# Kernel optimization log

Measured on AMD Instinct MI355X. Metric: run time of the kernel, lower is better.

The kernel has to match this reference:

```python
import jax, jax.numpy as jnp
import numpy as np

N_NODES = 100000
N_EDGES = 1600000
ATOM_EMB = 64
BOND_EMB = 16
MSG_DIM = 64
OUT_HIDDEN = 128
N_MOLS = 2048
MSG_PASSES = 4


def setup_inputs() -> dict:
    key = jax.random.key(0)
    ks = jax.random.split(key, 16)
    x = jax.random.randint(ks[0], (N_NODES,), 0, 119)
    edge_attr = jax.random.randint(ks[1], (N_EDGES,), 0, 4)
    edge_index = jax.random.randint(ks[2], (2, N_EDGES), 0, N_NODES)
    batch = jnp.sort(jax.random.randint(ks[3], (N_NODES,), 0, N_MOLS))
    s = 0.02
    atom_table = jax.random.normal(ks[4], (119, ATOM_EMB), jnp.float32) * s
    bond_table = jax.random.normal(ks[5], (4, BOND_EMB), jnp.float32) * s
    Wi = jax.random.normal(ks[6], (ATOM_EMB + BOND_EMB, MSG_DIM), jnp.float32) * s
    bi = jnp.zeros((MSG_DIM,), jnp.float32)
    Wu = jax.random.normal(ks[7], (ATOM_EMB + BOND_EMB + MSG_DIM, MSG_DIM), jnp.float32) * s
    bu = jnp.zeros((MSG_DIM,), jnp.float32)
    W1 = jax.random.normal(ks[8], (MSG_DIM, OUT_HIDDEN), jnp.float32) * s
    b1 = jnp.zeros((OUT_HIDDEN,), jnp.float32)
    W2 = jax.random.normal(ks[9], (OUT_HIDDEN, 1), jnp.float32) * s
    b2 = jnp.zeros((1,), jnp.float32)
    return {"x": x, "edge_attr": edge_attr, "edge_index": edge_index, "batch": batch,
            "atom_table": atom_table, "bond_table": bond_table,
            "Wi": Wi, "bi": bi, "Wu": Wu, "bu": bu,
            "W1": W1, "b1": b1, "W2": W2, "b2": b2}


def reference(x, edge_attr, edge_index, batch, atom_table, bond_table, Wi, bi, Wu, bu, W1, b1, W2, b2):
    atom = atom_table[x]                      # [N, ATOM_EMB]
    bond = bond_table[edge_attr]              # [E, BOND_EMB]
    src, dst = edge_index[0], edge_index[1]
    atom_src = atom[src]                      # [E, ATOM_EMB]
    ab = jnp.concatenate([atom_src, bond], axis=1)
    msg = jax.nn.relu(ab @ Wi + bi)           # [E, MSG_DIM]
    for _ in range(MSG_PASSES):
        agg = jax.ops.segment_sum(msg, dst, num_segments=N_NODES)  # [N, MSG_DIM]
        upd_in = jnp.concatenate([ab, agg[src]], axis=1)           # [E, 144]
        msg = jax.nn.relu(upd_in @ Wu + bu)
    node_state = jax.ops.segment_sum(msg, dst, num_segments=N_NODES)
    mol_state = jax.ops.segment_sum(node_state, batch, num_segments=N_MOLS)
    h = jax.nn.relu(mol_state @ W1 + b1)
    return (h @ W2 + b2).squeeze(-1)          # [N_MOLS]
```

## Files before the change

kernel.cpp:

```cpp
#include <hip/hip_runtime.h>

#define MSG 64
#define SLICE_SHIFT 10
#define MAXSLICES 128
#define CAP_E 20480
#define CAP_B 16384
#define NBIN 64

typedef _Float16 h2 __attribute__((ext_vector_type(2)));
typedef _Float16 h4 __attribute__((ext_vector_type(4)));
typedef _Float16 h8 __attribute__((ext_vector_type(8)));

__device__ inline h8 relu8(h8 v) {
    h8 z = {};
    return __builtin_elementwise_max(v, z);
}

__device__ inline h2 u2h(unsigned u) { union { unsigned u; h2 h; } c; c.u = u; return c.h; }

__global__ void build_tabA_kernel(const float* __restrict__ atom, const float* __restrict__ W,
                                  _Float16* __restrict__ tA, int rows) {
    int t = blockIdx.x * blockDim.x + threadIdx.x;
    if (t >= rows * MSG) return;
    int i = t & 63, a = t >> 6;
    float s = 0.f;
    for (int k = 0; k < 64; ++k) s = fmaf(atom[a * 64 + k], W[k * 64 + i], s);
    tA[t] = (_Float16)s;
}

__global__ void build_tabB_kernel(const float* __restrict__ bond, const float* __restrict__ W16,
                                  const float* __restrict__ bias, _Float16* __restrict__ tB) {
    int t = threadIdx.x;
    int i = t & 63, b = t >> 6;
    float s = bias[i];
    for (int k = 0; k < 16; ++k) s = fmaf(bond[b * 16 + k], W16[k * 64 + i], s);
    tB[t] = (_Float16)s;
}

__global__ void build_tabW_kernel(const float* __restrict__ W, unsigned* __restrict__ wst) {
    int t = blockIdx.x * 256 + threadIdx.x;
    if (t >= 2048) return;
    int k2 = t >> 6, c = t & 63;
    h2 h; h[0] = (_Float16)W[(2 * k2) * 64 + c]; h[1] = (_Float16)W[(2 * k2 + 1) * 64 + c];
    union { h2 h; unsigned u; } cv; cv.h = h;
    wst[k2 * 64 + c] = cv.u;
}

__global__ void node_init_kernel(const int* __restrict__ x, const _Float16* __restrict__ tA,
                                 _Float16* __restrict__ bufC, int N) {
    int t = blockIdx.x * blockDim.x + threadIdx.x;
    int v = t >> 3, j = t & 7;
    if (v < N) ((h8*)bufC)[(long long)v * 8 + j] = ((const h8*)tA)[x[v] * 8 + j];
}

__global__ void ginit_kernel(int* __restrict__ gcur, int K) {
    int s = blockIdx.x * blockDim.x + threadIdx.x;
    if (s < K) gcur[s] = s * CAP_E;
}

__global__ __launch_bounds__(256) void partition_kernel(
    const int* __restrict__ ei, const int* __restrict__ eattr,
    int E, int* __restrict__ gcur, unsigned long long* __restrict__ aux, int K)
{
    __shared__ int cnt[MAXSLICES];
    __shared__ int base[MAXSLICES];
    if (threadIdx.x < MAXSLICES) cnt[threadIdx.x] = 0;
    __syncthreads();
    int e0 = blockIdx.x * 1024;
    int sl0 = -1, sl1 = -1, sl2 = -1, sl3 = -1;
    int rk0 = 0, rk1 = 0, rk2 = 0, rk3 = 0;
    unsigned long long p0 = 0, p1 = 0, p2 = 0, p3 = 0;
    {
        int e = e0 + 0 * 256 + threadIdx.x;
        if (e < E) {
            int s = ei[e], d = ei[E + e];
            p0 = ((unsigned long long)((unsigned)s | ((unsigned)eattr[e] << 17)) << 17) | (unsigned)d;
            sl0 = d >> SLICE_SHIFT; rk0 = atomicAdd(&cnt[sl0], 1);
        }
    }
    {
        int e = e0 + 1 * 256 + threadIdx.x;
        if (e < E) {
            int s = ei[e], d = ei[E + e];
            p1 = ((unsigned long long)((unsigned)s | ((unsigned)eattr[e] << 17)) << 17) | (unsigned)d;
            sl1 = d >> SLICE_SHIFT; rk1 = atomicAdd(&cnt[sl1], 1);
        }
    }
    {
        int e = e0 + 2 * 256 + threadIdx.x;
        if (e < E) {
            int s = ei[e], d = ei[E + e];
            p2 = ((unsigned long long)((unsigned)s | ((unsigned)eattr[e] << 17)) << 17) | (unsigned)d;
            sl2 = d >> SLICE_SHIFT; rk2 = atomicAdd(&cnt[sl2], 1);
        }
    }
    {
        int e = e0 + 3 * 256 + threadIdx.x;
        if (e < E) {
            int s = ei[e], d = ei[E + e];
            p3 = ((unsigned long long)((unsigned)s | ((unsigned)eattr[e] << 17)) << 17) | (unsigned)d;
            sl3 = d >> SLICE_SHIFT; rk3 = atomicAdd(&cnt[sl3], 1);
        }
    }
    __syncthreads();
    if (threadIdx.x < K && cnt[threadIdx.x] > 0)
        base[threadIdx.x] = atomicAdd(&gcur[threadIdx.x], cnt[threadIdx.x]);
    __syncthreads();
    if (sl0 >= 0) aux[base[sl0] + rk0] = p0;
    if (sl1 >= 0) aux[base[sl1] + rk1] = p1;
    if (sl2 >= 0) aux[base[sl2] + rk2] = p2;
    if (sl3 >= 0) aux[base[sl3] + rk3] = p3;
}

__global__ __launch_bounds__(1024) void place_kernel(
    const unsigned long long* __restrict__ aux, const int* __restrict__ gcur,
    int* __restrict__ nstart, int* __restrict__ ndeg,
    unsigned* __restrict__ packed, int N)
{
    __shared__ int cnt[1 << SLICE_SHIFT];
    __shared__ int wsum[16];
    int s = blockIdx.x;
    int lo = s << SLICE_SHIFT;
    int start = s * CAP_E;
    int end = gcur[s];
    cnt[threadIdx.x] = 0;
    __syncthreads();
    for (int idx = start + threadIdx.x; idx < end; idx += 1024)
        atomicAdd(&cnt[(int)(aux[idx] & 0x1FFFFu) & ((1 << SLICE_SHIFT) - 1)], 1);
    __syncthreads();
    int c = cnt[threadIdx.x];
    int lane = threadIdx.x & 63, w = threadIdx.x >> 6;
    int sc = c;
    for (int off = 1; off < 64; off <<= 1) { int t = __shfl_up(sc, off); if (lane >= off) sc += t; }
    if (lane == 63) wsum[w] = sc;
    __syncthreads();
    if (w == 0 && lane < 16) {
        int t = wsum[lane];
        for (int off = 1; off < 16; off <<= 1) { int u = __shfl_up(t, off); if (lane >= off) t += u; }
        wsum[lane] = t;
    }
    __syncthreads();
    if (w > 0) sc += wsum[w - 1];
    int v = lo + threadIdx.x;
    int st = start + sc - c;
    if (v < N) { nstart[v] = st; ndeg[v] = c; }
    __syncthreads();
    cnt[threadIdx.x] = st;
    __syncthreads();
    for (int idx = start + threadIdx.x; idx < end; idx += 1024) {
        unsigned long long a = aux[idx];
        int d = (int)(a & 0x1FFFFu);
        unsigned pw = (unsigned)(a >> 17);
        int p = atomicAdd(&cnt[d & ((1 << SLICE_SHIFT) - 1)], 1);
        packed[p] = pw;
    }
}

__global__ __launch_bounds__(256) void dbin_kernel(const int* __restrict__ ndeg, int N,
                                                   int* __restrict__ bcnt, int* __restrict__ bucket) {
    __shared__ int cnt[NBIN];
    __shared__ int base[NBIN];
    if (threadIdx.x < NBIN) cnt[threadIdx.x] = 0;
    __syncthreads();
    int v = blockIdx.x * 256 + threadIdx.x;
    int b = -1, rk = 0;
    if (v < N) { b = min(ndeg[v], NBIN - 1); rk = atomicAdd(&cnt[b], 1); }
    __syncthreads();
    if (threadIdx.x < NBIN && cnt[threadIdx.x] > 0)
        base[threadIdx.x] = atomicAdd(&bcnt[threadIdx.x], cnt[threadIdx.x]);
    __syncthreads();
    if (b >= 0) bucket[b * CAP_B + base[b] + rk] = v;
}

__global__ void bscan_kernel(const int* __restrict__ bcnt, int* __restrict__ bbase) {
    if (threadIdx.x == 0 && blockIdx.x == 0) {
        int run = 0;
        for (int b = 0; b < NBIN; ++b) { bbase[b] = run; run += bcnt[b]; }
    }
}

__global__ void compact_kernel(const int* __restrict__ bucket, const int* __restrict__ bcnt,
                               const int* __restrict__ bbase, const int* __restrict__ nstart,
                               const int* __restrict__ ndeg, int2* __restrict__ srt) {
    int b = blockIdx.x;
    int n = bcnt[b], base = bbase[b];
    for (int i = threadIdx.x; i < n; i += 256) {
        int v = bucket[b * CAP_B + i];
        srt[base + i] = make_int2(nstart[v], v | (ndeg[v] << 17));
    }
}

template <bool FINAL>
__global__ __launch_bounds__(256) void gather_kernel(
    const unsigned* __restrict__ packed, const int2* __restrict__ srt,
    const _Float16* __restrict__ nodearr, const _Float16* __restrict__ tB,
    const unsigned* __restrict__ wst_g, const _Float16* __restrict__ tAu,
    const int* __restrict__ x, _Float16* __restrict__ out, int N)
{
    __shared__ _Float16 tbs[4 * 64];
    __shared__ unsigned wst[32 * 64];
    __shared__ _Float16 rowb[32][72];
    tbs[threadIdx.x] = tB[threadIdx.x];
    if (!FINAL)
        for (int idx = threadIdx.x; idx < 2048; idx += 256) wst[idx] = wst_g[idx];
    __syncthreads();
    int t = blockIdx.x * 256 + threadIdx.x;
    int vi = t >> 3;
    int j = threadIdx.x & 7;
    int w = threadIdx.x >> 3;
    const h8* na8 = (const h8*)nodearr;
    const _Float16* tbsj = tbs + j * 8;
    h8 acc = {};
    int v = 0;
    bool valid = vi < N;
    if (valid) {
        int2 s2 = srt[vi];
        int e = s2.x;
        v = (int)((unsigned)s2.y & 0x1FFFFu);
        int end = e + (int)((unsigned)s2.y >> 17);
        for (; e + 7 < end; e += 8) {
            unsigned q0 = packed[e],     q1 = packed[e + 1], q2 = packed[e + 2], q3 = packed[e + 3];
            unsigned q4 = packed[e + 4], q5 = packed[e + 5], q6 = packed[e + 6], q7 = packed[e + 7];
            h8 m0 = na8[(q0 & 0x1FFFFu) * 8 + j];
            h8 m1 = na8[(q1 & 0x1FFFFu) * 8 + j];
            h8 m2 = na8[(q2 & 0x1FFFFu) * 8 + j];
            h8 m3 = na8[(q3 & 0x1FFFFu) * 8 + j];
            h8 m4 = na8[(q4 & 0x1FFFFu) * 8 + j];
            h8 m5 = na8[(q5 & 0x1FFFFu) * 8 + j];
            h8 m6 = na8[(q6 & 0x1FFFFu) * 8 + j];
            h8 m7 = na8[(q7 & 0x1FFFFu) * 8 + j];
            h8 t0 = *(const h8*)&tbsj[(q0 >> 17) * 64];
            h8 t1 = *(const h8*)&tbsj[(q1 >> 17) * 64];
            h8 t2 = *(const h8*)&tbsj[(q2 >> 17) * 64];
            h8 t3 = *(const h8*)&tbsj[(q3 >> 17) * 64];
            h8 t4 = *(const h8*)&tbsj[(q4 >> 17) * 64];
            h8 t5 = *(const h8*)&tbsj[(q5 >> 17) * 64];
            h8 t6 = *(const h8*)&tbsj[(q6 >> 17) * 64];
            h8 t7 = *(const h8*)&tbsj[(q7 >> 17) * 64];
            h8 s0 = relu8(m0 + t0), s1 = relu8(m1 + t1);
            h8 s2v = relu8(m2 + t2), s3 = relu8(m3 + t3);
            h8 s4 = relu8(m4 + t4), s5 = relu8(m5 + t5);
            h8 s6 = relu8(m6 + t6), s7 = relu8(m7 + t7);
            acc += ((s0 + s1) + (s2v + s3)) + ((s4 + s5) + (s6 + s7));
        }
        for (; e < end; ++e) {
            unsigned q0 = packed[e];
            h8 m0 = na8[(q0 & 0x1FFFFu) * 8 + j];
            h8 t0 = *(const h8*)&tbsj[(q0 >> 17) * 64];
            acc += relu8(m0 + t0);
        }
    }
    if (FINAL) {
        if (valid) ((h8*)out)[(long long)v * 8 + j] = acc;
        return;
    }
    *(h8*)&rowb[w][j * 8] = acc;
    __syncthreads();
    if (!valid) return;
    const h2* rp = (const h2*)&rowb[w][0];
    const unsigned* wj = wst + j * 8;
    float o0 = 0.f, o1 = 0.f, o2 = 0.f, o3 = 0.f, o4 = 0.f, o5 = 0.f, o6 = 0.f, o7 = 0.f;
#pragma unroll
    for (int k2 = 0; k2 < 32; ++k2) {
        h2 r = rp[k2];
        uint4 wa = *(const uint4*)&wj[k2 * 64];
        uint4 wb = *(const uint4*)&wj[k2 * 64 + 4];
        o0 = __builtin_amdgcn_fdot2(r, u2h(wa.x), o0, false);
        o1 = __builtin_amdgcn_fdot2(r, u2h(wa.y), o1, false);
        o2 = __builtin_amdgcn_fdot2(r, u2h(wa.z), o2, false);
        o3 = __builtin_amdgcn_fdot2(r, u2h(wa.w), o3, false);
        o4 = __builtin_amdgcn_fdot2(r, u2h(wb.x), o4, false);
        o5 = __builtin_amdgcn_fdot2(r, u2h(wb.y), o5, false);
        o6 = __builtin_amdgcn_fdot2(r, u2h(wb.z), o6, false);
        o7 = __builtin_amdgcn_fdot2(r, u2h(wb.w), o7, false);
    }
    h8 ta = ((const h8*)tAu)[x[v] * 8 + j];
    h8 o;
    o[0] = (_Float16)(o0 + (float)ta[0]); o[1] = (_Float16)(o1 + (float)ta[1]);
    o[2] = (_Float16)(o2 + (float)ta[2]); o[3] = (_Float16)(o3 + (float)ta[3]);
    o[4] = (_Float16)(o4 + (float)ta[4]); o[5] = (_Float16)(o5 + (float)ta[5]);
    o[6] = (_Float16)(o6 + (float)ta[6]); o[7] = (_Float16)(o7 + (float)ta[7]);
    ((h8*)out)[(long long)v * 8 + j] = o;
}

__global__ void mol_pool_kernel(const _Float16* __restrict__ ns, const int* __restrict__ batch,
                                float* __restrict__ mol, int N) {
    int g = (blockIdx.x * blockDim.x + threadIdx.x) >> 4;
    int j = threadIdx.x & 15;
    int n0 = g * 32;
    if (n0 >= N) return;
    int n1 = min(n0 + 32, N);
    const h4* ns4 = (const h4*)ns;
    int cur = batch[n0];
    float ax = 0.f, ay = 0.f, az = 0.f, aw = 0.f;
    for (int n = n0; n < n1; ++n) {
        int b = batch[n];
        if (b != cur) {
            float* mp = &mol[(long long)cur * 64 + j * 4];
            atomicAdd(mp + 0, ax); atomicAdd(mp + 1, ay);
            atomicAdd(mp + 2, az); atomicAdd(mp + 3, aw);
            ax = ay = az = aw = 0.f; cur = b;
        }
        h4 vv = ns4[(long long)n * 16 + j];
        ax += (float)vv.x; ay += (float)vv.y; az += (float)vv.z; aw += (float)vv.w;
    }
    float* mp = &mol[(long long)cur * 64 + j * 4];
    atomicAdd(mp + 0, ax); atomicAdd(mp + 1, ay);
    atomicAdd(mp + 2, az); atomicAdd(mp + 3, aw);
}

__global__ void head_kernel(const float* __restrict__ mol, const float* __restrict__ W1,
                            const float* __restrict__ b1, const float* __restrict__ W2,
                            const float* __restrict__ b2, float* __restrict__ out) {
    int g = blockIdx.x;
    int j = threadIdx.x;
    float s = b1[j];
#pragma unroll
    for (int k = 0; k < 64; ++k) s = fmaf(mol[g * 64 + k], W1[k * 128 + j], s);
    s = fmaxf(s, 0.0f) * W2[j];
    __shared__ float red[128];
    red[j] = s;
    __syncthreads();
    for (int off = 64; off > 0; off >>= 1) {
        if (j < off) red[j] += red[j + off];
        __syncthreads();
    }
    if (j == 0) out[g] = red[0] + b2[0];
}

extern "C" void kernel_launch(void* const* d_in, const int* in_sizes, int n_in,
                              void* d_out, int out_size, void* d_ws, size_t ws_size,
                              hipStream_t stream) {
    const int*   x          = (const int*)d_in[0];
    const int*   eattr      = (const int*)d_in[1];
    const int*   ei         = (const int*)d_in[2];
    const int*   batch      = (const int*)d_in[3];
    const float* atom_table = (const float*)d_in[4];
    const float* bond_table = (const float*)d_in[5];
    const float* Wi         = (const float*)d_in[6];
    const float* bi         = (const float*)d_in[7];
    const float* Wu         = (const float*)d_in[8];
    const float* bu         = (const float*)d_in[9];
    const float* W1         = (const float*)d_in[10];
    const float* b1         = (const float*)d_in[11];
    const float* W2         = (const float*)d_in[12];
    const float* b2         = (const float*)d_in[13];

    const int N = in_sizes[0];
    const int E = in_sizes[1];
    const int M = out_size;
    const int AR = in_sizes[4] / 64;
    const int K = (N + (1 << SLICE_SHIFT) - 1) >> SLICE_SHIFT;

    char* ws = (char*)d_ws;
    size_t off_b = 0;
    auto alloc = [&](size_t bytes) -> void* {
        void* p = ws + off_b;
        off_b = (off_b + bytes + 255) & ~(size_t)255;
        return p;
    };
    size_t nbytes = (size_t)N * MSG * 2;
    size_t abytes = (size_t)K * CAP_E * 8;
    _Float16* bufA  = (_Float16*)alloc(nbytes);
    _Float16* bufB  = (_Float16*)alloc(nbytes > abytes ? nbytes : abytes);
    _Float16* bufC  = (_Float16*)alloc(nbytes);
    unsigned long long* aux = (unsigned long long*)bufB;
    unsigned* packed = (unsigned*)alloc((size_t)K * CAP_E * 4);
    int*      nstart = (int*)alloc((size_t)N * 4);
    int*      ndeg   = (int*)alloc((size_t)N * 4);
    int2*     srt    = (int2*)alloc((size_t)N * 8);
    int*      bucket = (int*)alloc((size_t)NBIN * CAP_B * 4);
    int*      bcnt   = (int*)alloc((size_t)NBIN * 4);
    int*      bbase  = (int*)alloc((size_t)NBIN * 4);
    int*      gcur   = (int*)alloc((size_t)MAXSLICES * 4);
    _Float16* tAi    = (_Float16*)alloc((size_t)AR * MSG * 2);
    _Float16* tBi    = (_Float16*)alloc((size_t)4 * MSG * 2);
    _Float16* tAu    = (_Float16*)alloc((size_t)AR * MSG * 2);
    _Float16* tBu    = (_Float16*)alloc((size_t)4 * MSG * 2);
    unsigned* wstb   = (unsigned*)alloc((size_t)32 * 64 * 4);
    float*    mol    = (float*)alloc((size_t)M * MSG * 4);
    (void)ws_size; (void)n_in;

    const float* Wagg = Wu + 80 * MSG;
    build_tabA_kernel<<<(AR * MSG + 255) / 256, 256, 0, stream>>>(atom_table, Wi, tAi, AR);
    build_tabB_kernel<<<1, 256, 0, stream>>>(bond_table, Wi + 64 * MSG, bi, tBi);
    build_tabA_kernel<<<(AR * MSG + 255) / 256, 256, 0, stream>>>(atom_table, Wu, tAu, AR);
    build_tabB_kernel<<<1, 256, 0, stream>>>(bond_table, Wu + 64 * MSG, bu, tBu);
    build_tabW_kernel<<<8, 256, 0, stream>>>(Wagg, wstb);
    node_init_kernel<<<(int)(((long long)N * 8 + 255) / 256), 256, 0, stream>>>(x, tAi, bufC, N);

    ginit_kernel<<<1, MAXSLICES, 0, stream>>>(gcur, K);
    partition_kernel<<<(E + 1023) / 1024, 256, 0, stream>>>(ei, eattr, E, gcur, aux, K);
    place_kernel<<<K, 1024, 0, stream>>>(aux, gcur, nstart, ndeg, packed, N);

    hipMemsetAsync(bcnt, 0, (size_t)NBIN * 4, stream);
    dbin_kernel<<<(N + 255) / 256, 256, 0, stream>>>(ndeg, N, bcnt, bucket);
    bscan_kernel<<<1, 64, 0, stream>>>(bcnt, bbase);
    compact_kernel<<<NBIN, 256, 0, stream>>>(bucket, bcnt, bbase, nstart, ndeg, srt);

    const int gblocks = (int)(((long long)N * 8 + 255) / 256);
    gather_kernel<false><<<gblocks, 256, 0, stream>>>(packed, srt, bufC, tBi, wstb, tAu, x, bufA, N);
    gather_kernel<false><<<gblocks, 256, 0, stream>>>(packed, srt, bufA, tBu, wstb, tAu, x, bufB, N);
    gather_kernel<false><<<gblocks, 256, 0, stream>>>(packed, srt, bufB, tBu, wstb, tAu, x, bufA, N);
    gather_kernel<false><<<gblocks, 256, 0, stream>>>(packed, srt, bufA, tBu, wstb, tAu, x, bufB, N);
    gather_kernel<true><<<gblocks, 256, 0, stream>>>(packed, srt, bufB, tBu, nullptr, nullptr, nullptr, bufA, N);

    hipMemsetAsync(mol, 0, (size_t)M * MSG * 4, stream);
    mol_pool_kernel<<<(((N + 31) / 32) * 16 + 255) / 256, 256, 0, stream>>>(bufA, batch, mol, N);
    head_kernel<<<M, 128, 0, stream>>>(mol, W1, b1, W2, b2, (float*)d_out);
}
```

Before: 313.6 us.

## Merge setup kernels, shard partition counters, fold scan into compact, bound gather occupancy

Folds the five table-building kernels and the counter init into one setup launch, and removes the separate bucket-scan kernel by having each compact block sum the preceding bucket counts itself. The partition step now spreads its global atomic counters over eight replicas per slice so fewer blocks contend on the same address, and the place kernel walks all replicas. The gather kernel gets a launch bound asking for eight blocks per unit, which may force register spilling. The per-replica capacity of 3072 edges is a fixed assumption and could overflow on skewed inputs.

```diff
diff --git a/kernel.cpp b/kernel.cpp
--- a/kernel.cpp
+++ b/kernel.cpp
@@ -3,6 +3,8 @@
 #define MSG 64
 #define SLICE_SHIFT 10
 #define MAXSLICES 128
+#define REP 8
+#define CAP_R 3072
 #define CAP_E 20480
 #define CAP_B 16384
 #define NBIN 64
@@ -18,32 +20,49 @@
 
 __device__ inline h2 u2h(unsigned u) { union { unsigned u; h2 h; } c; c.u = u; return c.h; }
 
-__global__ void build_tabA_kernel(const float* __restrict__ atom, const float* __restrict__ W,
-                                  _Float16* __restrict__ tA, int rows) {
-    int t = blockIdx.x * blockDim.x + threadIdx.x;
-    if (t >= rows * MSG) return;
-    int i = t & 63, a = t >> 6;
-    float s = 0.f;
-    for (int k = 0; k < 64; ++k) s = fmaf(atom[a * 64 + k], W[k * 64 + i], s);
-    tA[t] = (_Float16)s;
-}
-
-__global__ void build_tabB_kernel(const float* __restrict__ bond, const float* __restrict__ W16,
-                                  const float* __restrict__ bias, _Float16* __restrict__ tB) {
-    int t = threadIdx.x;
-    int i = t & 63, b = t >> 6;
-    float s = bias[i];
-    for (int k = 0; k < 16; ++k) s = fmaf(bond[b * 16 + k], W16[k * 64 + i], s);
-    tB[t] = (_Float16)s;
-}
-
-__global__ void build_tabW_kernel(const float* __restrict__ W, unsigned* __restrict__ wst) {
-    int t = blockIdx.x * 256 + threadIdx.x;
-    if (t >= 2048) return;
-    int k2 = t >> 6, c = t & 63;
-    h2 h; h[0] = (_Float16)W[(2 * k2) * 64 + c]; h[1] = (_Float16)W[(2 * k2 + 1) * 64 + c];
-    union { h2 h; unsigned u; } cv; cv.h = h;
-    wst[k2 * 64 + c] = cv.u;
+__global__ void setup_kernel(const float* __restrict__ atom, const float* __restrict__ bond,
+                             const float* __restrict__ Wi, const float* __restrict__ bi,
+                             const float* __restrict__ Wu, const float* __restrict__ bu,
+                             const float* __restrict__ Wagg,
+                             _Float16* __restrict__ tAi, _Float16* __restrict__ tBi,
+                             _Float16* __restrict__ tAu, _Float16* __restrict__ tBu,
+                             unsigned* __restrict__ wst, int* __restrict__ gcur,
+                             int AR, int K, int ab) {
+    int b = blockIdx.x;
+    if (b < 2 * ab + 2) {
+        bool upd = b >= ab + 1;
+        const float* W = upd ? Wu : Wi;
+        int lb = upd ? b - (ab + 1) : b;
+        if (lb < ab) {
+            _Float16* tA = upd ? tAu : tAi;
+            int t = lb * 256 + threadIdx.x;
+            if (t < AR * MSG) {
+                int i = t & 63, a = t >> 6;
+                float s = 0.f;
+                for (int k = 0; k < 64; ++k) s = fmaf(atom[a * 64 + k], W[k * 64 + i], s);
+                tA[t] = (_Float16)s;
+            }
+        } else {
+            _Float16* tBo = upd ? tBu : tBi;
+            const float* bias = upd ? bu : bi;
+            const float* W16 = W + 64 * MSG;
+            int t = threadIdx.x;
+            int i = t & 63, r = t >> 6;
+            float s = bias[i];
+            for (int k = 0; k < 16; ++k) s = fmaf(bond[r * 16 + k], W16[k * 64 + i], s);
+            tBo[t] = (_Float16)s;
+        }
+    } else if (b < 2 * ab + 10) {
+        int t = (b - (2 * ab + 2)) * 256 + threadIdx.x;
+        if (t < 2048) {
+            int k2 = t >> 6, c = t & 63;
+            h2 h; h[0] = (_Float16)Wagg[(2 * k2) * 64 + c]; h[1] = (_Float16)Wagg[(2 * k2 + 1) * 64 + c];
+            union { h2 h; unsigned u; } cv; cv.h = h;
+            wst[k2 * 64 + c] = cv.u;
+        }
+    } else {
+        for (int q = threadIdx.x; q < K * REP; q += 256) gcur[q] = q * CAP_R;
+    }
 }
 
 __global__ void node_init_kernel(const int* __restrict__ x, const _Float16* __restrict__ tA,
@@ -51,11 +70,6 @@
     int t = blockIdx.x * blockDim.x + threadIdx.x;
     int v = t >> 3, j = t & 7;
     if (v < N) ((h8*)bufC)[(long long)v * 8 + j] = ((const h8*)tA)[x[v] * 8 + j];
-}
-
-__global__ void ginit_kernel(int* __restrict__ gcur, int K) {
-    int s = blockIdx.x * blockDim.x + threadIdx.x;
-    if (s < K) gcur[s] = s * CAP_E;
 }
 
 __global__ __launch_bounds__(256) void partition_kernel(
@@ -66,6 +80,7 @@
     __shared__ int base[MAXSLICES];
     if (threadIdx.x < MAXSLICES) cnt[threadIdx.x] = 0;
     __syncthreads();
+    int rep = blockIdx.x & (REP - 1);
     int e0 = blockIdx.x * 1024;
     int sl0 = -1, sl1 = -1, sl2 = -1, sl3 = -1;
     int rk0 = 0, rk1 = 0, rk2 = 0, rk3 = 0;
@@ -104,7 +119,7 @@
     }
     __syncthreads();
     if (threadIdx.x < K && cnt[threadIdx.x] > 0)
-        base[threadIdx.x] = atomicAdd(&gcur[threadIdx.x], cnt[threadIdx.x]);
+        base[threadIdx.x] = atomicAdd(&gcur[threadIdx.x * REP + rep], cnt[threadIdx.x]);
     __syncthreads();
     if (sl0 >= 0) aux[base[sl0] + rk0] = p0;
     if (sl1 >= 0) aux[base[sl1] + rk1] = p1;
@@ -121,12 +136,14 @@
     __shared__ int wsum[16];
     int s = blockIdx.x;
     int lo = s << SLICE_SHIFT;
-    int start = s * CAP_E;
-    int end = gcur[s];
     cnt[threadIdx.x] = 0;
     __syncthreads();
-    for (int idx = start + threadIdx.x; idx < end; idx += 1024)
-        atomicAdd(&cnt[(int)(aux[idx] & 0x1FFFFu) & ((1 << SLICE_SHIFT) - 1)], 1);
+    for (int r = 0; r < REP; ++r) {
+        int q = s * REP + r;
+        int start = q * CAP_R, end = gcur[q];
+        for (int idx = start + threadIdx.x; idx < end; idx += 1024)
+            atomicAdd(&cnt[(int)(aux[idx] & 0x1FFFFu) & ((1 << SLICE_SHIFT) - 1)], 1);
+    }
     __syncthreads();
     int c = cnt[threadIdx.x];
     int lane = threadIdx.x & 63, w = threadIdx.x >> 6;
@@ -142,17 +159,21 @@
     __syncthreads();
     if (w > 0) sc += wsum[w - 1];
     int v = lo + threadIdx.x;
-    int st = start + sc - c;
+    int st = s * CAP_E + sc - c;
     if (v < N) { nstart[v] = st; ndeg[v] = c; }
     __syncthreads();
     cnt[threadIdx.x] = st;
     __syncthreads();
-    for (int idx = start + threadIdx.x; idx < end; idx += 1024) {
-        unsigned long long a = aux[idx];
-        int d = (int)(a & 0x1FFFFu);
-        unsigned pw = (unsigned)(a >> 17);
-        int p = atomicAdd(&cnt[d & ((1 << SLICE_SHIFT) - 1)], 1);
-        packed[p] = pw;
+    for (int r = 0; r < REP; ++r) {
+        int q = s * REP + r;
+        int start = q * CAP_R, end = gcur[q];
+        for (int idx = start + threadIdx.x; idx < end; idx += 1024) {
+            unsigned long long a = aux[idx];
+            int d = (int)(a & 0x1FFFFu);
+            unsigned pw = (unsigned)(a >> 17);
+            int p = atomicAdd(&cnt[d & ((1 << SLICE_SHIFT) - 1)], 1);
+            packed[p] = pw;
+        }
     }
 }
 
@@ -172,18 +193,18 @@
     if (b >= 0) bucket[b * CAP_B + base[b] + rk] = v;
 }
 
-__global__ void bscan_kernel(const int* __restrict__ bcnt, int* __restrict__ bbase) {
-    if (threadIdx.x == 0 && blockIdx.x == 0) {
+__global__ void compact_kernel(const int* __restrict__ bucket, const int* __restrict__ bcnt,
+                               const int* __restrict__ nstart, const int* __restrict__ ndeg,
+                               int2* __restrict__ srt) {
+    __shared__ int sbase;
+    int b = blockIdx.x;
+    if (threadIdx.x == 0) {
         int run = 0;
-        for (int b = 0; b < NBIN; ++b) { bbase[b] = run; run += bcnt[b]; }
-    }
-}
-
-__global__ void compact_kernel(const int* __restrict__ bucket, const int* __restrict__ bcnt,
-                               const int* __restrict__ bbase, const int* __restrict__ nstart,
-                               const int* __restrict__ ndeg, int2* __restrict__ srt) {
-    int b = blockIdx.x;
-    int n = bcnt[b], base = bbase[b];
+        for (int i = 0; i < b; ++i) run += bcnt[i];
+        sbase = run;
+    }
+    __syncthreads();
+    int n = bcnt[b], base = sbase;
     for (int i = threadIdx.x; i < n; i += 256) {
         int v = bucket[b * CAP_B + i];
         srt[base + i] = make_int2(nstart[v], v | (ndeg[v] << 17));
@@ -191,7 +212,7 @@
 }
 
 template <bool FINAL>
-__global__ __launch_bounds__(256) void gather_kernel(
+__global__ __launch_bounds__(256, 8) void gather_kernel(
     const unsigned* __restrict__ packed, const int2* __restrict__ srt,
     const _Float16* __restrict__ nodearr, const _Float16* __restrict__ tB,
     const unsigned* __restrict__ wst_g, const _Float16* __restrict__ tAu,
@@ -351,6 +372,7 @@
     const int M = out_size;
     const int AR = in_sizes[4] / 64;
     const int K = (N + (1 << SLICE_SHIFT) - 1) >> SLICE_SHIFT;
+    const int ab = (AR * MSG + 255) / 256;
 
     char* ws = (char*)d_ws;
     size_t off_b = 0;
@@ -360,7 +382,7 @@
         return p;
     };
     size_t nbytes = (size_t)N * MSG * 2;
-    size_t abytes = (size_t)K * CAP_E * 8;
+    size_t abytes = (size_t)K * REP * CAP_R * 8;
     _Float16* bufA  = (_Float16*)alloc(nbytes);
     _Float16* bufB  = (_Float16*)alloc(nbytes > abytes ? nbytes : abytes);
     _Float16* bufC  = (_Float16*)alloc(nbytes);
@@ -371,8 +393,7 @@
     int2*     srt    = (int2*)alloc((size_t)N * 8);
     int*      bucket = (int*)alloc((size_t)NBIN * CAP_B * 4);
     int*      bcnt   = (int*)alloc((size_t)NBIN * 4);
-    int*      bbase  = (int*)alloc((size_t)NBIN * 4);
-    int*      gcur   = (int*)alloc((size_t)MAXSLICES * 4);
+    int*      gcur   = (int*)alloc((size_t)MAXSLICES * REP * 4);
     _Float16* tAi    = (_Float16*)alloc((size_t)AR * MSG * 2);
     _Float16* tBi    = (_Float16*)alloc((size_t)4 * MSG * 2);
     _Float16* tAu    = (_Float16*)alloc((size_t)AR * MSG * 2);
@@ -382,21 +403,17 @@
     (void)ws_size; (void)n_in;
 
     const float* Wagg = Wu + 80 * MSG;
-    build_tabA_kernel<<<(AR * MSG + 255) / 256, 256, 0, stream>>>(atom_table, Wi, tAi, AR);
-    build_tabB_kernel<<<1, 256, 0, stream>>>(bond_table, Wi + 64 * MSG, bi, tBi);
-    build_tabA_kernel<<<(AR * MSG + 255) / 256, 256, 0, stream>>>(atom_table, Wu, tAu, AR);
-    build_tabB_kernel<<<1, 256, 0, stream>>>(bond_table, Wu + 64 * MSG, bu, tBu);
-    build_tabW_kernel<<<8, 256, 0, stream>>>(Wagg, wstb);
+
+    setup_kernel<<<2 * ab + 11, 256, 0, stream>>>(atom_table, bond_table, Wi, bi, Wu, bu, Wagg,
+                                                  tAi, tBi, tAu, tBu, wstb, gcur, AR, K, ab);
     node_init_kernel<<<(int)(((long long)N * 8 + 255) / 256), 256, 0, stream>>>(x, tAi, bufC, N);
 
-    ginit_kernel<<<1, MAXSLICES, 0, stream>>>(gcur, K);
     partition_kernel<<<(E + 1023) / 1024, 256, 0, stream>>>(ei, eattr, E, gcur, aux, K);
     place_kernel<<<K, 1024, 0, stream>>>(aux, gcur, nstart, ndeg, packed, N);
 
     hipMemsetAsync(bcnt, 0, (size_t)NBIN * 4, stream);
     dbin_kernel<<<(N + 255) / 256, 256, 0, stream>>>(ndeg, N, bcnt, bucket);
-    bscan_kernel<<<1, 64, 0, stream>>>(bcnt, bbase);
-    compact_kernel<<<NBIN, 256, 0, stream>>>(bucket, bcnt, bbase, nstart, ndeg, srt);
+    compact_kernel<<<NBIN, 256, 0, stream>>>(bucket, bcnt, nstart, ndeg, srt);
 
     const int gblocks = (int)(((long long)N * 8 + 255) / 256);
     gather_kernel<false><<<gblocks, 256, 0, stream>>>(packed, srt, bufC, tBi, wstb, tAu, x, bufA, N);
```

Result: faster. 304.3 us (-3.0%).
